# Optimization experiments

Hardware: AMD Instinct MI355X
Metric: run time of the kernel (lower is better)

Reference implementation:

```python
import jax, jax.numpy as jnp
import numpy as np

EPS = 1e-6
N_HEADS = 16


def _inner(x, y):
    # Lorentzian inner product: -x0*y0 + <x_space, y_space>
    return -x[..., 0] * y[..., 0] + jnp.sum(x[..., 1:] * y[..., 1:], axis=-1)


def _project(x):
    sp = jnp.clip(x[..., 1:], -8.0, 8.0)
    x0 = jnp.sqrt(1.0 + jnp.sum(sp ** 2, axis=-1, keepdims=True) + EPS)
    return jnp.concatenate([x0, sp], axis=-1)


def _exp_map(x, v):
    vx = _inner(v, x)[..., None]
    v_tan = v + vx * x
    v_ns = jnp.maximum(_inner(v_tan, v_tan), 0.0)
    v_n = jnp.minimum(jnp.sqrt(v_ns + EPS)[..., None], 5.0)
    res = jnp.cosh(v_n) * x + jnp.sinh(v_n) * v_tan / (v_n + EPS)
    return _project(res)


def _log_map(x, y):
    y = _project(y)
    xy = jnp.minimum(_inner(x, y)[..., None], -(1.0 + EPS))
    d = jnp.maximum(jnp.arccosh(jnp.maximum(-xy, 1.0 + EPS)), 0.001)
    direc = y + xy * x
    dn = jnp.sqrt(jnp.maximum(_inner(direc, direc), EPS))[..., None]
    return d * direc / (dn + EPS)


def setup_inputs() -> dict:
    key = jax.random.key(0)
    ks = jax.random.split(key, 5)
    B, T, d = 2, 1024, 1024
    x = jax.random.normal(ks[0], (B, T, d), dtype=jnp.float32)
    s = 0.02
    Wq = jax.random.normal(ks[1], (d, d), dtype=jnp.float32) * s
    Wk = jax.random.normal(ks[2], (d, d), dtype=jnp.float32) * s
    Wv = jax.random.normal(ks[3], (d, d), dtype=jnp.float32) * s
    Wo = jax.random.normal(ks[4], (d, d), dtype=jnp.float32) * s
    return {"x": x, "Wq": Wq, "Wk": Wk, "Wv": Wv, "Wo": Wo}


def reference(x, Wq, Wk, Wv, Wo):
    B, T, d = x.shape
    h = N_HEADS
    dh = d // h
    mu = jnp.zeros((d,), dtype=x.dtype).at[0].set(1.0)  # hyperboloid origin

    v = _log_map(mu, x)  # [B, T, d]

    def proj_h(w):
        hh = w.reshape(B, T, h, dh)
        sp = jnp.clip(hh[..., 1:], -5.0, 5.0)
        x0 = jnp.sqrt(1.0 + jnp.sum(sp ** 2, axis=-1, keepdims=True) + EPS)
        return jnp.transpose(jnp.concatenate([x0, sp], axis=-1), (0, 2, 1, 3))  # [B,h,T,dh]

    q = proj_h(v @ Wq.T)
    k = proj_h(v @ Wk.T)
    vv = jnp.transpose((v @ Wv.T).reshape(B, T, h, dh), (0, 2, 1, 3))  # [B,h,T,dh]

    # Lorentzian scores: -q0*k0 + <q_space, k_space>
    sc = (-jnp.einsum("bhqi,bhki->bhqk", q[..., :1], k[..., :1])
          + jnp.einsum("bhqc,bhkc->bhqk", q[..., 1:], k[..., 1:])) / (dh ** 0.5)
    at = jax.nn.softmax(sc, axis=-1)
    out = jnp.einsum("bhqk,bhkc->bhqc", at, vv)
    out = jnp.transpose(out, (0, 2, 1, 3)).reshape(B, T, d)
    return _project(_exp_map(mu, out @ Wo.T))
```

## Files before the change

### kernel.cpp

```cpp
#include <hip/hip_runtime.h>

#define EPSF 1e-6f

typedef __bf16 bf16x8 __attribute__((ext_vector_type(8)));
typedef float f32x4 __attribute__((ext_vector_type(4)));
typedef __attribute__((address_space(3))) unsigned int as3_uint;
typedef __attribute__((address_space(1))) const unsigned int as1_uint;

__device__ __forceinline__ unsigned short f2bf(float f) {
  unsigned int u = __builtin_bit_cast(unsigned int, f);
  u += 0x7fffu + ((u >> 16) & 1u);
  return (unsigned short)(u >> 16);
}
__device__ __forceinline__ float bf2f(unsigned short u) {
  unsigned int v = (unsigned int)u << 16;
  return __builtin_bit_cast(float, v);
}

__global__ __launch_bounds__(256) void prep_and_conv(
    const float* __restrict__ x, const float* __restrict__ Wq,
    const float* __restrict__ Wk, const float* __restrict__ Wv,
    const float* __restrict__ Wo, unsigned short* __restrict__ vbf,
    unsigned short* __restrict__ wqk, unsigned short* __restrict__ wvb,
    unsigned short* __restrict__ wob) {
  int bid = blockIdx.x;
  int tid = threadIdx.x;
  if (bid >= 2048) {
    int t = bid - 2048;
    int y = t >> 10;
    const float* src = (y == 0) ? Wq : (y == 1) ? Wk : (y == 2) ? Wv : Wo;
    unsigned short* dst = (y == 0) ? wqk : (y == 1) ? wqk + 1048576
                          : (y == 2) ? wvb : wob;
    int i = (t & 1023) * 256 + tid;
    f32x4 v = ((const f32x4*)src)[i];
    ushort4 o;
    o.x = f2bf(v[0]); o.y = f2bf(v[1]); o.z = f2bf(v[2]); o.w = f2bf(v[3]);
    ((ushort4*)dst)[i] = o;
    return;
  }
  int row = bid;
  const float* xr = x + (size_t)row * 1024;
  float vals[4];
  float ssq = 0.f;
#pragma unroll
  for (int i = 0; i < 4; ++i) {
    int c = tid + i * 256;
    float t = xr[c];
    if (c == 0) {
      vals[i] = 0.f;
    } else {
      t = fminf(fmaxf(t, -8.f), 8.f);
      vals[i] = t;
      ssq += t * t;
    }
  }
#pragma unroll
  for (int off = 32; off; off >>= 1) ssq += __shfl_xor(ssq, off);
  __shared__ float red[4];
  int wv = tid >> 6;
  if ((tid & 63) == 0) red[wv] = ssq;
  __syncthreads();
  ssq = red[0] + red[1] + red[2] + red[3];

  float y0 = sqrtf(1.f + ssq + EPSF);
  float xy = fminf(-y0, -(1.f + EPSF));
  float mxy = fmaxf(-xy, 1.f + EPSF);
  float dd = fmaxf(acoshf(mxy), 0.001f);
  float d0 = y0 + xy;
  float inn = ssq - d0 * d0;
  float dn = sqrtf(fmaxf(inn, EPSF));
  float inv = dd / (dn + EPSF);

  unsigned short* vr = vbf + (size_t)row * 1024;
#pragma unroll
  for (int i = 0; i < 4; ++i) {
    int c = tid + i * 256;
    float o = (c == 0) ? d0 * inv : vals[i] * inv;
    vr[c] = f2bf(o);
  }
}

__device__ __forceinline__ void gemm128_body(
    const unsigned short* __restrict__ A, const unsigned short* __restrict__ Bw,
    int K, int row0, int col0, unsigned short* As, unsigned short* Bs,
    f32x4 (*acc)[4]) {
  int tid = threadIdx.x;
  int lane = tid & 63, w = tid >> 6;
  int wm = (w >> 1) * 64, wn = (w & 1) * 64;
  int lq = lane & 15, g = lane >> 4;
  const unsigned short* Ag =
      A + (size_t)(row0 + w * 8 + (lane >> 3)) * K + (lane & 7) * 8;
  const unsigned short* Bg =
      Bw + (size_t)(col0 + w * 8 + (lane >> 3)) * K + (lane & 7) * 8;

  for (int k0 = 0; k0 < K; k0 += 64) {
    __syncthreads();
#pragma unroll
    for (int it = 0; it < 4; ++it) {
      __builtin_amdgcn_global_load_lds(
          (as1_uint*)(Ag + (size_t)(it * 32) * K + k0),
          (as3_uint*)&As[(it * 32 + w * 8) * 64], 16, 0, 0);
      __builtin_amdgcn_global_load_lds(
          (as1_uint*)(Bg + (size_t)(it * 32) * K + k0),
          (as3_uint*)&Bs[(it * 32 + w * 8) * 64], 16, 0, 0);
    }
    __syncthreads();
#pragma unroll
    for (int ks = 0; ks < 2; ++ks) {
      bf16x8 af[4], bfr[4];
#pragma unroll
      for (int i = 0; i < 4; ++i)
        af[i] = *(const bf16x8*)&As[(wm + i * 16 + lq) * 64 + ks * 32 + g * 8];
#pragma unroll
      for (int j = 0; j < 4; ++j)
        bfr[j] = *(const bf16x8*)&Bs[(wn + j * 16 + lq) * 64 + ks * 32 + g * 8];
#pragma unroll
      for (int i = 0; i < 4; ++i)
#pragma unroll
        for (int j = 0; j < 4; ++j)
          acc[i][j] =
              __builtin_amdgcn_mfma_f32_16x16x32_bf16(af[i], bfr[j], acc[i][j], 0, 0, 0);
    }
  }
}

__global__ __launch_bounds__(256) void gemm_qkv(
    const unsigned short* __restrict__ vbf, const unsigned short* __restrict__ wqk,
    const unsigned short* __restrict__ wvb, unsigned short* __restrict__ qb,
    unsigned short* __restrict__ kb, unsigned short* __restrict__ vtb) {
  __shared__ unsigned short As[128 * 64];
  __shared__ unsigned short Bs[128 * 64];
  f32x4 acc[4][4] = {};
  int tid = threadIdx.x;
  int lane = tid & 63, w = tid >> 6;
  int wm = (w >> 1) * 64, wn = (w & 1) * 64;
  int lq = lane & 15, g = lane >> 4;
  int bid = blockIdx.x;

  if (bid < 256) {
    int row0 = (bid & 15) * 128, col0 = (bid >> 4) * 128;
    gemm128_body(vbf, wqk, 1024, row0, col0, As, Bs, acc);
    int headg = (col0 + wn) >> 6;
    int qmode = (headg < 16) ? 1 : 0;
    unsigned short* dst = qmode ? qb : kb;
    size_t colb = (size_t)(headg & 15) * 64;
    float scale = qmode ? 0.125f : 1.f;
#pragma unroll
    for (int i = 0; i < 4; ++i)
#pragma unroll
      for (int r = 0; r < 4; ++r) {
        float s = 0.f;
#pragma unroll
        for (int j = 0; j < 4; ++j) {
          float vc = fminf(fmaxf(acc[i][j][r], -5.f), 5.f);
          s += (j == 0 && lq == 0) ? 0.f : vc * vc;
        }
        s += __shfl_xor(s, 1);
        s += __shfl_xor(s, 2);
        s += __shfl_xor(s, 4);
        s += __shfl_xor(s, 8);
        float x0 = sqrtf(1.f + s + EPSF);
        int row = row0 + wm + i * 16 + g * 4 + r;
#pragma unroll
        for (int j = 0; j < 4; ++j) {
          float vc = fminf(fmaxf(acc[i][j][r], -5.f), 5.f);
          float o = (j == 0 && lq == 0) ? (qmode ? -x0 : x0) : vc;
          dst[(size_t)row * 1024 + colb + j * 16 + lq] = f2bf(o * scale);
        }
      }
  } else {
    int t = bid - 256;
    int row0 = (t & 7) * 128, col0 = (t >> 3) * 128;
    gemm128_body(wvb, vbf, 1024, row0, col0, As, Bs, acc);
#pragma unroll
    for (int i = 0; i < 4; ++i)
#pragma unroll
      for (int j = 0; j < 4; ++j)
#pragma unroll
        for (int r = 0; r < 4; ++r)
          vtb[(size_t)(row0 + wm + i * 16 + g * 4 + r) * 2048 + col0 + wn + j * 16 + lq] =
              f2bf(acc[i][j][r]);
  }
}

__global__ __launch_bounds__(256) void gemm_wo(
    const unsigned short* __restrict__ A, const unsigned short* __restrict__ Bw,
    unsigned short* __restrict__ C) {
  __shared__ unsigned short As[128 * 64];
  __shared__ unsigned short Bs[64 * 64];
  int tid = threadIdx.x;
  int lane = tid & 63, w = tid >> 6;
  int wm = (w >> 1) * 64, wn = (w & 1) * 32;
  int lq = lane & 15, g = lane >> 4;
  int row0 = (blockIdx.x & 15) * 128, col0 = (blockIdx.x >> 4) * 64;
  f32x4 acc[4][2] = {};
  const unsigned short* Ag =
      A + (size_t)(row0 + w * 8 + (lane >> 3)) * 1024 + (lane & 7) * 8;
  const unsigned short* Bg =
      Bw + (size_t)(col0 + w * 8 + (lane >> 3)) * 1024 + (lane & 7) * 8;

  for (int k0 = 0; k0 < 1024; k0 += 64) {
    __syncthreads();
#pragma unroll
    for (int it = 0; it < 4; ++it)
      __builtin_amdgcn_global_load_lds(
          (as1_uint*)(Ag + (size_t)(it * 32) * 1024 + k0),
          (as3_uint*)&As[(it * 32 + w * 8) * 64], 16, 0, 0);
#pragma unroll
    for (int it = 0; it < 2; ++it)
      __builtin_amdgcn_global_load_lds(
          (as1_uint*)(Bg + (size_t)(it * 32) * 1024 + k0),
          (as3_uint*)&Bs[(it * 32 + w * 8) * 64], 16, 0, 0);
    __syncthreads();
#pragma unroll
    for (int ks = 0; ks < 2; ++ks) {
      bf16x8 af[4], bfr[2];
#pragma unroll
      for (int i = 0; i < 4; ++i)
        af[i] = *(const bf16x8*)&As[(wm + i * 16 + lq) * 64 + ks * 32 + g * 8];
#pragma unroll
      for (int j = 0; j < 2; ++j)
        bfr[j] = *(const bf16x8*)&Bs[(wn + j * 16 + lq) * 64 + ks * 32 + g * 8];
#pragma unroll
      for (int i = 0; i < 4; ++i)
#pragma unroll
        for (int j = 0; j < 2; ++j)
          acc[i][j] =
              __builtin_amdgcn_mfma_f32_16x16x32_bf16(af[i], bfr[j], acc[i][j], 0, 0, 0);
    }
  }
#pragma unroll
  for (int i = 0; i < 4; ++i)
#pragma unroll
    for (int j = 0; j < 2; ++j)
#pragma unroll
      for (int r = 0; r < 4; ++r)
        C[(size_t)(row0 + wm + i * 16 + g * 4 + r) * 1024 + col0 + wn + j * 16 + lq] =
            f2bf(acc[i][j][r]);
}

__global__ __launch_bounds__(256) void attn_mfma(
    const unsigned short* __restrict__ Qb, const unsigned short* __restrict__ Kb,
    const unsigned short* __restrict__ Vtb, unsigned short* __restrict__ Obf) {
  __shared__ unsigned short Ks[2][64 * 64];
  __shared__ unsigned short Vs[2][64 * 64];
  __shared__ unsigned short Ps[4 * 16 * 64];
  int tid = threadIdx.x;
  int lane = tid & 63, w = tid >> 6;
  int g = lane >> 4, lq = lane & 15;
  int bid = blockIdx.x;
  int idx = bid >> 3;
  int bh = (bid & 7) * 4 + (idx & 3);
  int qt = idx >> 2;
  int b = bh >> 4, h = bh & 15;

  const unsigned short* qrow =
      Qb + (size_t)(b * 1024 + qt * 64 + w * 16 + lq) * 1024 + h * 64;
  bf16x8 qf0 = *(const bf16x8*)(qrow + g * 8);
  bf16x8 qf1 = *(const bf16x8*)(qrow + 32 + g * 8);

  float mreg = -1e30f, lreg = 0.f;
  f32x4 acc[4] = {};
  unsigned short* Pw = Ps + w * 16 * 64;
  int sx = 8 * (lq & 7);

  const unsigned short* Ksrc = Kb + (size_t)(b * 1024) * 1024 + h * 64;
  const unsigned short* Vsrc = Vtb + (size_t)(h * 64) * 2048 + b * 1024;

  int srow = lane >> 3;
  int scg = (lane & 7) ^ srow;
  const unsigned short* Kp = Ksrc + (size_t)(w * 8 + srow) * 1024 + scg * 8;
  const unsigned short* Vp = Vsrc + (size_t)(w * 8 + srow) * 2048 + scg * 8;

  auto stage = [&](int buf, int kt) {
#pragma unroll
    for (int it = 0; it < 2; ++it) {
      __builtin_amdgcn_global_load_lds(
          (as1_uint*)(Kp + (size_t)(kt * 64 + it * 32) * 1024),
          (as3_uint*)&Ks[buf][(it * 32 + w * 8) * 64], 16, 0, 0);
      __builtin_amdgcn_global_load_lds(
          (as1_uint*)(Vp + (size_t)(it * 32) * 2048 + kt * 64),
          (as3_uint*)&Vs[buf][(it * 32 + w * 8) * 64], 16, 0, 0);
    }
  };

  auto compute = [&](int buf) {
    f32x4 st[4];
    __builtin_amdgcn_s_setprio(1);
#pragma unroll
    for (int i = 0; i < 4; ++i) {
      int ro = i * 16 + lq;
      int rb = ro * 64, xx = 8 * (ro & 7);
      bf16x8 a0 = *(const bf16x8*)&Ks[buf][rb + ((g * 8) ^ xx)];
      bf16x8 a1 = *(const bf16x8*)&Ks[buf][rb + ((32 + g * 8) ^ xx)];
      f32x4 z = {};
      z = __builtin_amdgcn_mfma_f32_16x16x32_bf16(a0, qf0, z, 0, 0, 0);
      st[i] = __builtin_amdgcn_mfma_f32_16x16x32_bf16(a1, qf1, z, 0, 0, 0);
    }
    __builtin_amdgcn_s_setprio(0);
    float pmax = st[0][0];
#pragma unroll
    for (int i = 0; i < 4; ++i)
#pragma unroll
      for (int r = 0; r < 4; ++r) pmax = fmaxf(pmax, st[i][r]);
    pmax = fmaxf(pmax, __shfl_xor(pmax, 16));
    pmax = fmaxf(pmax, __shfl_xor(pmax, 32));
    if (__any(pmax > mreg + 8.f)) {
      float nm = fmaxf(mreg, pmax);
      float sc_ = __expf(mreg - nm);
      mreg = nm;
      lreg *= sc_;
      float scr[4];
#pragma unroll
      for (int r = 0; r < 4; ++r) scr[r] = __shfl(sc_, g * 4 + r);
#pragma unroll
      for (int jj = 0; jj < 4; ++jj)
#pragma unroll
        for (int r = 0; r < 4; ++r) acc[jj][r] *= scr[r];
    }
    float ps = 0.f;
#pragma unroll
    for (int i = 0; i < 4; ++i) {
      ushort4 pq;
      float p0 = __expf(st[i][0] - mreg);
      float p1 = __expf(st[i][1] - mreg);
      float p2 = __expf(st[i][2] - mreg);
      float p3 = __expf(st[i][3] - mreg);
      ps += (p0 + p1) + (p2 + p3);
      pq.x = f2bf(p0); pq.y = f2bf(p1); pq.z = f2bf(p2); pq.w = f2bf(p3);
      *(ushort4*)&Pw[lq * 64 + ((g * 4 + i * 16) ^ sx)] = pq;
    }
    ps += __shfl_xor(ps, 16);
    ps += __shfl_xor(ps, 32);
    lreg += ps;

    __builtin_amdgcn_s_setprio(1);
#pragma unroll
    for (int ks = 0; ks < 2; ++ks) {
      bf16x8 pa = *(const bf16x8*)&Pw[lq * 64 + ((ks * 32 + g * 8) ^ sx)];
#pragma unroll
      for (int jj = 0; jj < 4; ++jj) {
        int vr = 16 * jj + lq;
        bf16x8 vb = *(const bf16x8*)&Vs[buf][vr * 64 + ((ks * 32 + g * 8) ^ (8 * (vr & 7)))];
        acc[jj] = __builtin_amdgcn_mfma_f32_16x16x32_bf16(pa, vb, acc[jj], 0, 0, 0);
      }
    }
    __builtin_amdgcn_s_setprio(0);
  };

  stage(0, 0);
  int buf = 0;
  for (int kt = 0; kt < 16; ++kt) {
    __syncthreads();
    if (kt + 1 < 16) stage(buf ^ 1, kt + 1);
    compute(buf);
    buf ^= 1;
  }

  float linv = 1.f / lreg;
  float ilr[4];
#pragma unroll
  for (int r = 0; r < 4; ++r) ilr[r] = __shfl(linv, g * 4 + r);
  unsigned short* obase =
      Obf + (size_t)(b * 1024 + qt * 64 + w * 16) * 1024 + h * 64;
#pragma unroll
  for (int r = 0; r < 4; ++r)
#pragma unroll
    for (int jj = 0; jj < 4; ++jj)
      obase[(size_t)(g * 4 + r) * 1024 + 16 * jj + lq] = f2bf(acc[jj][r] * ilr[r]);
}

__global__ __launch_bounds__(256) void expmap_project(
    const unsigned short* __restrict__ c2, float* __restrict__ out) {
  int row = blockIdx.x;
  int tid = threadIdx.x;
  const unsigned short* cr = c2 + (size_t)row * 1024;
  float vals[4];
  float ssq = 0.f;
#pragma unroll
  for (int i = 0; i < 4; ++i) {
    int c = tid + i * 256;
    float t = bf2f(cr[c]);
    vals[i] = (c == 0) ? 0.f : t;
    ssq += vals[i] * vals[i];
  }
#pragma unroll
  for (int off = 32; off; off >>= 1) ssq += __shfl_xor(ssq, off);
  __shared__ float red1[4], red2[4];
  int wv = tid >> 6;
  if ((tid & 63) == 0) red1[wv] = ssq;
  __syncthreads();
  ssq = red1[0] + red1[1] + red1[2] + red1[3];
  float vn = fminf(sqrtf(ssq + EPSF), 5.f);
  float bf = sinhf(vn) / (vn + EPSF);
  float s2 = 0.f;
#pragma unroll
  for (int i = 0; i < 4; ++i) {
    float r = fminf(fmaxf(bf * vals[i], -8.f), 8.f);
    vals[i] = r;
    s2 += r * r;
  }
#pragma unroll
  for (int off = 32; off; off >>= 1) s2 += __shfl_xor(s2, off);
  if ((tid & 63) == 0) red2[wv] = s2;
  __syncthreads();
  s2 = red2[0] + red2[1] + red2[2] + red2[3];
  float x0 = sqrtf(1.f + s2 + EPSF);
  float* orow = out + (size_t)row * 1024;
#pragma unroll
  for (int i = 0; i < 4; ++i) {
    int c = tid + i * 256;
    orow[c] = (c == 0) ? x0 : vals[i];
  }
}

extern "C" void kernel_launch(void* const* d_in, const int* in_sizes, int n_in,
                              void* d_out, int out_size, void* d_ws, size_t ws_size,
                              hipStream_t stream) {
  (void)in_sizes; (void)n_in; (void)out_size; (void)ws_size;
  const float* x  = (const float*)d_in[0];
  const float* Wq = (const float*)d_in[1];
  const float* Wk = (const float*)d_in[2];
  const float* Wv = (const float*)d_in[3];
  const float* Wo = (const float*)d_in[4];
  float* out = (float*)d_out;

  char* w = (char*)d_ws;
  unsigned short* vbf = (unsigned short*)w; w += (size_t)2048 * 1024 * 2;
  unsigned short* wqk = (unsigned short*)w; w += (size_t)2048 * 1024 * 2;
  unsigned short* wvb = (unsigned short*)w; w += (size_t)1024 * 1024 * 2;
  unsigned short* wob = (unsigned short*)w; w += (size_t)1024 * 1024 * 2;
  unsigned short* vtb = (unsigned short*)w; w += (size_t)1024 * 2048 * 2;
  unsigned short* qb  = (unsigned short*)w; w += (size_t)2048 * 1024 * 2;
  unsigned short* kb  = (unsigned short*)w; w += (size_t)2048 * 1024 * 2;
  unsigned short* aob = (unsigned short*)w; w += (size_t)2048 * 1024 * 2;
  unsigned short* c2  = (unsigned short*)w; w += (size_t)2048 * 1024 * 2;

  prep_and_conv<<<6144, 256, 0, stream>>>(x, Wq, Wk, Wv, Wo, vbf, wqk, wvb, wob);

  gemm_qkv<<<384, 256, 0, stream>>>(vbf, wqk, wvb, qb, kb, vtb);

  attn_mfma<<<512, 256, 0, stream>>>(qb, kb, vtb, aob);

  gemm_wo<<<256, 256, 0, stream>>>(aob, wob, c2);
  expmap_project<<<2048, 256, 0, stream>>>(c2, out);
}
```

Before: 84.78 us.

## Double-buffer LDS tiles in QKV and Wo GEMMs and interleave V blocks

Both projection GEMMs now keep two LDS buffers. The next K-slice is prefetched with global_load_lds while MFMAs run on the current slice, which removes one barrier per iteration and hides global load latency. The QKV launch also spreads the V-transpose blocks among the Q/K blocks (every third block id) so heavier and lighter tiles share CUs more evenly. The cost is doubled LDS per block (64KB for QKV), which may reduce occupancy. Correctness also relies on the barrier waiting for outstanding LDS-DMA loads.

After: 84.20 us. About the same (-0.7%).

```diff
diff --git a/kernel.cpp b/kernel.cpp
--- a/kernel.cpp
+++ b/kernel.cpp
@@ -80,7 +80,7 @@
   }
 }
 
-__device__ __forceinline__ void gemm128_body(
+__device__ __forceinline__ void gemm128_dbuf(
     const unsigned short* __restrict__ A, const unsigned short* __restrict__ Bw,
     int K, int row0, int col0, unsigned short* As, unsigned short* Bs,
     f32x4 (*acc)[4]) {
@@ -93,27 +93,32 @@
   const unsigned short* Bg =
       Bw + (size_t)(col0 + w * 8 + (lane >> 3)) * K + (lane & 7) * 8;
 
+  auto stage = [&](int buf, int k0) {
+#pragma unroll
+    for (int it = 0; it < 4; ++it) {
+      __builtin_amdgcn_global_load_lds(
+          (as1_uint*)(Ag + (size_t)(it * 32) * K + k0),
+          (as3_uint*)&As[buf * 8192 + (it * 32 + w * 8) * 64], 16, 0, 0);
+      __builtin_amdgcn_global_load_lds(
+          (as1_uint*)(Bg + (size_t)(it * 32) * K + k0),
+          (as3_uint*)&Bs[buf * 8192 + (it * 32 + w * 8) * 64], 16, 0, 0);
+    }
+  };
+
+  stage(0, 0);
+  int buf = 0;
   for (int k0 = 0; k0 < K; k0 += 64) {
     __syncthreads();
-#pragma unroll
-    for (int it = 0; it < 4; ++it) {
-      __builtin_amdgcn_global_load_lds(
-          (as1_uint*)(Ag + (size_t)(it * 32) * K + k0),
-          (as3_uint*)&As[(it * 32 + w * 8) * 64], 16, 0, 0);
-      __builtin_amdgcn_global_load_lds(
-          (as1_uint*)(Bg + (size_t)(it * 32) * K + k0),
-          (as3_uint*)&Bs[(it * 32 + w * 8) * 64], 16, 0, 0);
-    }
-    __syncthreads();
+    if (k0 + 64 < K) stage(buf ^ 1, k0 + 64);
 #pragma unroll
     for (int ks = 0; ks < 2; ++ks) {
       bf16x8 af[4], bfr[4];
 #pragma unroll
       for (int i = 0; i < 4; ++i)
-        af[i] = *(const bf16x8*)&As[(wm + i * 16 + lq) * 64 + ks * 32 + g * 8];
+        af[i] = *(const bf16x8*)&As[buf * 8192 + (wm + i * 16 + lq) * 64 + ks * 32 + g * 8];
 #pragma unroll
       for (int j = 0; j < 4; ++j)
-        bfr[j] = *(const bf16x8*)&Bs[(wn + j * 16 + lq) * 64 + ks * 32 + g * 8];
+        bfr[j] = *(const bf16x8*)&Bs[buf * 8192 + (wn + j * 16 + lq) * 64 + ks * 32 + g * 8];
 #pragma unroll
       for (int i = 0; i < 4; ++i)
 #pragma unroll
@@ -121,6 +126,7 @@
           acc[i][j] =
               __builtin_amdgcn_mfma_f32_16x16x32_bf16(af[i], bfr[j], acc[i][j], 0, 0, 0);
     }
+    buf ^= 1;
   }
 }
 
@@ -128,18 +134,20 @@
     const unsigned short* __restrict__ vbf, const unsigned short* __restrict__ wqk,
     const unsigned short* __restrict__ wvb, unsigned short* __restrict__ qb,
     unsigned short* __restrict__ kb, unsigned short* __restrict__ vtb) {
-  __shared__ unsigned short As[128 * 64];
-  __shared__ unsigned short Bs[128 * 64];
+  __shared__ unsigned short As[2 * 8192];
+  __shared__ unsigned short Bs[2 * 8192];
   f32x4 acc[4][4] = {};
   int tid = threadIdx.x;
   int lane = tid & 63, w = tid >> 6;
   int wm = (w >> 1) * 64, wn = (w & 1) * 64;
   int lq = lane & 15, g = lane >> 4;
   int bid = blockIdx.x;
-
-  if (bid < 256) {
-    int row0 = (bid & 15) * 128, col0 = (bid >> 4) * 128;
-    gemm128_body(vbf, wqk, 1024, row0, col0, As, Bs, acc);
+  bool isVt = (bid % 3 == 2);
+
+  if (!isVt) {
+    int q = bid - (bid + 1) / 3;
+    int row0 = (q & 15) * 128, col0 = (q >> 4) * 128;
+    gemm128_dbuf(vbf, wqk, 1024, row0, col0, As, Bs, acc);
     int headg = (col0 + wn) >> 6;
     int qmode = (headg < 16) ? 1 : 0;
     unsigned short* dst = qmode ? qb : kb;
@@ -169,9 +177,9 @@
         }
       }
   } else {
-    int t = bid - 256;
+    int t = bid / 3;
     int row0 = (t & 7) * 128, col0 = (t >> 3) * 128;
-    gemm128_body(wvb, vbf, 1024, row0, col0, As, Bs, acc);
+    gemm128_dbuf(wvb, vbf, 1024, row0, col0, As, Bs, acc);
 #pragma unroll
     for (int i = 0; i < 4; ++i)
 #pragma unroll
@@ -186,8 +194,8 @@
 __global__ __launch_bounds__(256) void gemm_wo(
     const unsigned short* __restrict__ A, const unsigned short* __restrict__ Bw,
     unsigned short* __restrict__ C) {
-  __shared__ unsigned short As[128 * 64];
-  __shared__ unsigned short Bs[64 * 64];
+  __shared__ unsigned short As[2 * 8192];
+  __shared__ unsigned short Bs[2 * 4096];
   int tid = threadIdx.x;
   int lane = tid & 63, w = tid >> 6;
   int wm = (w >> 1) * 64, wn = (w & 1) * 32;
@@ -199,28 +207,33 @@
   const unsigned short* Bg =
       Bw + (size_t)(col0 + w * 8 + (lane >> 3)) * 1024 + (lane & 7) * 8;
 
+  auto stage = [&](int buf, int k0) {
+#pragma unroll
+    for (int it = 0; it < 4; ++it)
+      __builtin_amdgcn_global_load_lds(
+          (as1_uint*)(Ag + (size_t)(it * 32) * 1024 + k0),
+          (as3_uint*)&As[buf * 8192 + (it * 32 + w * 8) * 64], 16, 0, 0);
+#pragma unroll
+    for (int it = 0; it < 2; ++it)
+      __builtin_amdgcn_global_load_lds(
+          (as1_uint*)(Bg + (size_t)(it * 32) * 1024 + k0),
+          (as3_uint*)&Bs[buf * 4096 + (it * 32 + w * 8) * 64], 16, 0, 0);
+  };
+
+  stage(0, 0);
+  int buf = 0;
   for (int k0 = 0; k0 < 1024; k0 += 64) {
     __syncthreads();
-#pragma unroll
-    for (int it = 0; it < 4; ++it)
-      __builtin_amdgcn_global_load_lds(
-          (as1_uint*)(Ag + (size_t)(it * 32) * 1024 + k0),
-          (as3_uint*)&As[(it * 32 + w * 8) * 64], 16, 0, 0);
-#pragma unroll
-    for (int it = 0; it < 2; ++it)
-      __builtin_amdgcn_global_load_lds(
-          (as1_uint*)(Bg + (size_t)(it * 32) * 1024 + k0),
-          (as3_uint*)&Bs[(it * 32 + w * 8) * 64], 16, 0, 0);
-    __syncthreads();
+    if (k0 + 64 < 1024) stage(buf ^ 1, k0 + 64);
 #pragma unroll
     for (int ks = 0; ks < 2; ++ks) {
       bf16x8 af[4], bfr[2];
 #pragma unroll
       for (int i = 0; i < 4; ++i)
-        af[i] = *(const bf16x8*)&As[(wm + i * 16 + lq) * 64 + ks * 32 + g * 8];
+        af[i] = *(const bf16x8*)&As[buf * 8192 + (wm + i * 16 + lq) * 64 + ks * 32 + g * 8];
 #pragma unroll
       for (int j = 0; j < 2; ++j)
-        bfr[j] = *(const bf16x8*)&Bs[(wn + j * 16 + lq) * 64 + ks * 32 + g * 8];
+        bfr[j] = *(const bf16x8*)&Bs[buf * 4096 + (wn + j * 16 + lq) * 64 + ks * 32 + g * 8];
 #pragma unroll
       for (int i = 0; i < 4; ++i)
 #pragma unroll
@@ -228,6 +241,7 @@
           acc[i][j] =
               __builtin_amdgcn_mfma_f32_16x16x32_bf16(af[i], bfr[j], acc[i][j], 0, 0, 0);
     }
+    buf ^= 1;
   }
 #pragma unroll
   for (int i = 0; i < 4; ++i)
```
